# Kernel optimization log

Measured on AMD Instinct MI355X. Metric: run time of the kernel, lower is better.

## Reference

```python
import math
import jax, jax.numpy as jnp
import numpy as np

B, L, D, H = 2, 2048, 1024, 16
HD = D // H
EPS = 1e-6
ROPE_BASE = 10000.0


def setup_inputs() -> dict:
    key = jax.random.key(0)
    ks = jax.random.split(key, 6)
    s = 0.02
    return {
        "z_H_previous": jax.random.normal(ks[0], (B, L, D), jnp.float32),
        "z_L_current": jax.random.normal(ks[1], (B, L, D), jnp.float32),
        "w_qkv": jax.random.normal(ks[2], (3 * D, D), jnp.float32) * s,
        "w_out": jax.random.normal(ks[3], (D, D), jnp.float32) * s,
        "w_ffn1": jax.random.normal(ks[4], (4 * D, D), jnp.float32) * s,
        "w_ffn2": jax.random.normal(ks[5], (D, 4 * D), jnp.float32) * s,
        "g_norm1": jnp.ones((D,), jnp.float32),
        "g_norm2": jnp.ones((D,), jnp.float32),
    }


def _rmsnorm(x, g):
    # mean of squares over last dim, rsqrt, scale
    ms = jnp.mean(x * x, axis=-1, keepdims=True)
    return x * jax.lax.rsqrt(ms + EPS) * g


def _rope(x):
    # x: [b, h, l, hd]; non-interleaved rotate-half RoPE
    l, d = x.shape[-2], x.shape[-1]
    half = d // 2
    inv_freq = 1.0 / (ROPE_BASE ** (jnp.arange(half, dtype=jnp.float32) / half))
    freqs = jnp.arange(l, dtype=jnp.float32)[:, None] * inv_freq[None, :]  # [l, half]
    cos, sin = jnp.cos(freqs), jnp.sin(freqs)
    x1, x2 = x[..., :half], x[..., half:]
    return jnp.concatenate([x1 * cos - x2 * sin, x2 * cos + x1 * sin], axis=-1)


def reference(z_H_previous, z_L_current, w_qkv, w_out, w_ffn1, w_ffn2, g_norm1, g_norm2):
    x = z_H_previous + z_L_current                       # [b, l, d]
    h = _rmsnorm(x, g_norm1)
    b, l, d = h.shape
    qkv = h @ w_qkv.T                                    # [b, l, 3d]
    qkv = qkv.reshape(b, l, 3, H, HD).transpose(2, 0, 3, 1, 4)  # [3, b, h, l, hd]
    q, k, v = qkv[0], qkv[1], qkv[2]
    q = _rope(q)
    k = _rope(k)
    scores = jnp.einsum("bhqd,bhkd->bhqk", q, k) / math.sqrt(HD)
    attn = jax.nn.softmax(scores, axis=-1)
    out = jnp.einsum("bhqk,bhkd->bhqd", attn, v)         # [b, h, l, hd]
    out = out.transpose(0, 2, 1, 3).reshape(b, l, d)
    x = x + out @ w_out.T
    h2 = _rmsnorm(x, g_norm2)
    ffn = jax.nn.silu(h2 @ w_ffn1.T) @ w_ffn2.T
    return x + ffn
```

## Files before the change

### kernel.cpp

```cpp
#include <hip/hip_runtime.h>

typedef __bf16 bf16;
typedef __bf16 bf16x2 __attribute__((ext_vector_type(2)));
typedef __bf16 bf16x8 __attribute__((ext_vector_type(8)));
typedef __bf16 bf16x4 __attribute__((ext_vector_type(4)));
typedef float  f32x4  __attribute__((ext_vector_type(4)));
typedef float  f32x16 __attribute__((ext_vector_type(16)));
typedef unsigned int uint;

static __device__ __forceinline__ void async_copy16(const void* g, void* l) {
  __builtin_amdgcn_global_load_lds((__attribute__((address_space(1))) void*)g,
                                   (__attribute__((address_space(3))) void*)l,
                                   16, 0, 0);
}

static __device__ __forceinline__ uint pkbf2(float a, float b) {
  union { bf16x2 v; uint u; } x;
  x.v[0] = (bf16)a; x.v[1] = (bf16)b;
  return x.u;
}

union U4 { uint u[4]; bf16x8 v; };

__global__ __launch_bounds__(256) void f2b_kernel(const float* __restrict__ in,
                                                  bf16* __restrict__ out, int n4) {
  int i = blockIdx.x * 256 + threadIdx.x;
  if (i < n4) {
    float4 v = ((const float4*)in)[i];
    bf16x4 o;
    o[0] = (bf16)v.x; o[1] = (bf16)v.y; o[2] = (bf16)v.z; o[3] = (bf16)v.w;
    ((bf16x4*)out)[i] = o;
  }
}

__global__ __launch_bounds__(256)
void add_rmsnorm_kernel(const float* __restrict__ a, const float* __restrict__ b,
                        const float* __restrict__ g, float* __restrict__ xout,
                        bf16* __restrict__ hout) {
  const int row = blockIdx.x;
  const int tid = threadIdx.x;
  const size_t base = (size_t)row * 1024 + tid * 4;
  float4 x = *(const float4*)(a + base);
  if (b) {
    float4 y = *(const float4*)(b + base);
    x.x += y.x; x.y += y.y; x.z += y.z; x.w += y.w;
  }
  float ss = x.x*x.x + x.y*x.y + x.z*x.z + x.w*x.w;
#pragma unroll
  for (int off = 32; off > 0; off >>= 1) ss += __shfl_xor(ss, off, 64);
  __shared__ float red[4];
  const int wave = tid >> 6, lane = tid & 63;
  if (lane == 0) red[wave] = ss;
  __syncthreads();
  const float total = red[0] + red[1] + red[2] + red[3];
  const float scale = rsqrtf(total * (1.0f / 1024.0f) + 1e-6f);
  if (xout) *(float4*)(xout + base) = x;
  float4 gv = *(const float4*)(g + tid * 4);
  bf16x4 h;
  h[0] = (bf16)(x.x * scale * gv.x);
  h[1] = (bf16)(x.y * scale * gv.y);
  h[2] = (bf16)(x.z * scale * gv.z);
  h[3] = (bf16)(x.w * scale * gv.w);
  *(bf16x4*)(hout + base) = h;
}

__global__ __launch_bounds__(256) void rope_kernel(bf16* __restrict__ qk) {
  int idx = blockIdx.x * 256 + threadIdx.x;
  const int hd = idx & 31; idx >>= 5;
  const int l  = idx & 2047; idx >>= 11;
  const int h  = idx & 15; idx >>= 4;
  const int b  = idx & 1;  idx >>= 1;
  bf16* p = qk + (size_t)idx * 4194304 + ((size_t)(b * 16 + h) * 2048 + l) * 64;
  const float inv = powf(10000.0f, -(float)hd * (1.0f / 32.0f));
  const float fr = (float)l * inv;
  float s, c; sincosf(fr, &s, &c);
  const float x1 = (float)p[hd], x2 = (float)p[hd + 32];
  p[hd]      = (bf16)(x1 * c - x2 * s);
  p[hd + 32] = (bf16)(x2 * c + x1 * s);
}

enum { EP_QKV = 0, EP_ADD_RESID = 1, EP_SILU = 2 };

template <int MODE>
__global__ __launch_bounds__(256)
void gemm_bt(const bf16* __restrict__ A, const bf16* __restrict__ W,
             const float* __restrict__ resid, float* __restrict__ outF,
             bf16* __restrict__ outB, bf16* __restrict__ outB2,
             int M, int N, int K) {
  __shared__ bf16 As[128 * 32];
  __shared__ bf16 Bs[128 * 32];
  const int tid  = threadIdx.x;
  const int wave = tid >> 6;
  const int lane = tid & 63;
  const int quad = lane >> 4;
  const int l16  = lane & 15;

  const int nb = N >> 7;
  const int bm = blockIdx.x / nb;
  const int bn = blockIdx.x - bm * nb;
  const int m0 = bm << 7, n0 = bn << 7;
  const int wm = (wave >> 1) << 6;
  const int wn = (wave & 1) << 6;

  const int srow = wave * 32 + (lane >> 2);
  const int scol = (lane & 3) * 8;
  const bf16* gA = A + (size_t)(m0 + srow) * K + scol;
  const bf16* gB = W + (size_t)(n0 + srow) * K + scol;
  bf16* lA0 = &As[(wave * 32) * 32];
  bf16* lA1 = &As[(wave * 32 + 16) * 32];
  bf16* lB0 = &Bs[(wave * 32) * 32];
  bf16* lB1 = &Bs[(wave * 32 + 16) * 32];

  f32x4 acc[4][4] = {};

  for (int k0 = 0; k0 < K; k0 += 32) {
    __syncthreads();
    async_copy16(gA, lA0);
    async_copy16(gA + (size_t)16 * K, lA1);
    async_copy16(gB, lB0);
    async_copy16(gB + (size_t)16 * K, lB1);
    gA += 32; gB += 32;
    __syncthreads();
    bf16x8 af[4], bfr[4];
#pragma unroll
    for (int i = 0; i < 4; i++)
      af[i] = *(const bf16x8*)&As[(wm + i * 16 + l16) * 32 + quad * 8];
#pragma unroll
    for (int j = 0; j < 4; j++)
      bfr[j] = *(const bf16x8*)&Bs[(wn + j * 16 + l16) * 32 + quad * 8];
#pragma unroll
    for (int i = 0; i < 4; i++)
#pragma unroll
      for (int j = 0; j < 4; j++)
        acc[i][j] = __builtin_amdgcn_mfma_f32_16x16x32_bf16(af[i], bfr[j], acc[i][j], 0, 0, 0);
  }

#pragma unroll
  for (int i = 0; i < 4; i++) {
    const int mbase = m0 + wm + i * 16 + quad * 4;
#pragma unroll
    for (int j = 0; j < 4; j++) {
      const int n = n0 + wn + j * 16 + l16;
      f32x4 v = acc[i][j];
#pragma unroll
      for (int r = 0; r < 4; r++) {
        const int m = mbase + r;
        const float val = v[r];
        if constexpr (MODE == EP_QKV) {
          const int bb = m >> 11, l = m & 2047;
          const int which = n >> 10, hh = (n >> 6) & 15, hd = n & 63;
          if (which == 2) {
            outB2[((size_t)(bb * 16 + hh) * 64 + hd) * 2048 + l] = (bf16)val;
          } else {
            const float sc = (which == 0) ? 0.1803368801111243f : 1.0f;
            outB[(((size_t)(which * 2 + bb) * 16 + hh) * 2048 + l) * 64 + hd] = (bf16)(val * sc);
          }
        } else if constexpr (MODE == EP_ADD_RESID) {
          outF[(size_t)m * N + n] = val + resid[(size_t)m * N + n];
        } else {
          outB[(size_t)m * N + n] = (bf16)(val / (1.0f + __expf(-val)));
        }
      }
    }
  }
}

__global__ __launch_bounds__(256)
void gemm64_bt(const bf16* __restrict__ A, const bf16* __restrict__ W,
               const float* __restrict__ resid, float* __restrict__ outF,
               int M, int N, int K) {
  __shared__ bf16 As[64 * 32];
  __shared__ bf16 Bs[128 * 32];
  const int tid = threadIdx.x, wave = tid >> 6, lane = tid & 63;
  const int quad = lane >> 4, l16 = lane & 15;
  const int nb = N >> 7;
  const int bm = blockIdx.x / nb, bn = blockIdx.x - bm * nb;
  const int m0 = bm << 6, n0 = bn << 7;
  const int wm = (wave >> 1) * 32, wn = (wave & 1) * 64;

  const int arow = wave * 16 + (lane >> 2);
  const int brow = wave * 32 + (lane >> 2);
  const int scol = (lane & 3) * 8;
  const bf16* gA = A + (size_t)(m0 + arow) * K + scol;
  const bf16* gB = W + (size_t)(n0 + brow) * K + scol;
  bf16* lA  = &As[(wave * 16) * 32];
  bf16* lB0 = &Bs[(wave * 32) * 32];
  bf16* lB1 = &Bs[(wave * 32 + 16) * 32];

  f32x4 acc[2][4] = {};
  for (int k0 = 0; k0 < K; k0 += 32) {
    __syncthreads();
    async_copy16(gA, lA);
    async_copy16(gB, lB0);
    async_copy16(gB + (size_t)16 * K, lB1);
    gA += 32; gB += 32;
    __syncthreads();
    bf16x8 af[2], bfr[4];
#pragma unroll
    for (int i = 0; i < 2; i++)
      af[i] = *(const bf16x8*)&As[(wm + i * 16 + l16) * 32 + quad * 8];
#pragma unroll
    for (int j = 0; j < 4; j++)
      bfr[j] = *(const bf16x8*)&Bs[(wn + j * 16 + l16) * 32 + quad * 8];
#pragma unroll
    for (int i = 0; i < 2; i++)
#pragma unroll
      for (int j = 0; j < 4; j++)
        acc[i][j] = __builtin_amdgcn_mfma_f32_16x16x32_bf16(af[i], bfr[j], acc[i][j], 0, 0, 0);
  }
#pragma unroll
  for (int i = 0; i < 2; i++) {
    const int mbase = m0 + wm + i * 16 + quad * 4;
#pragma unroll
    for (int j = 0; j < 4; j++) {
      const int n = n0 + wn + j * 16 + l16;
#pragma unroll
      for (int r = 0; r < 4; r++) {
        const int m = mbase + r;
        outF[(size_t)m * N + n] = acc[i][j][r] + resid[(size_t)m * N + n];
      }
    }
  }
}

__global__ __launch_bounds__(256, 4)
void attn_kernel(const bf16* __restrict__ qk, const bf16* __restrict__ vt,
                 bf16* __restrict__ Opart, float* __restrict__ Lpart) {
  const int qt    = blockIdx.x & 15;
  const int bh    = (blockIdx.x >> 4) & 31;
  const int split = blockIdx.x >> 9;
  const bf16* Qp = qk + (size_t)bh * 131072;
  const bf16* Kp = Qp + 4194304;
  const bf16* Vp = vt + (size_t)bh * 131072;

  const int tid = threadIdx.x, wave = tid >> 6, lane = tid & 63;
  const int hl = lane >> 5, l32 = lane & 31;
  const int qw = qt * 128 + wave * 32;

  __shared__ bf16 lds[9216];
  bf16* Ks = lds;
  bf16* Vs = lds + 4096;

  bf16x8 qf[4];
#pragma unroll
  for (int dk = 0; dk < 4; dk++)
    qf[dk] = *(const bf16x8*)&Qp[(size_t)(qw + l32) * 64 + dk * 16 + hl * 8];

  f32x16 o0 = {}, o1 = {};
  float l_i = 0.0f;

  const int rl = lane >> 3;
  const int cg = (lane & 7) ^ rl;

  const int kvbase = split * 512;
  for (int kv0 = kvbase; kv0 < kvbase + 512; kv0 += 64) {
    __syncthreads();
#pragma unroll
    for (int i = 0; i < 2; i++) {
      const int row = wave * 16 + i * 8;
      async_copy16(Kp + (size_t)(kv0 + row + rl) * 64 + cg * 8, &Ks[row * 64]);
      async_copy16(Vp + (size_t)(row + rl) * 2048 + kv0 + cg * 8, &Vs[row * 64]);
    }
    __syncthreads();

    f32x16 s0 = {}, s1 = {};
#pragma unroll
    for (int dk = 0; dk < 4; dk++) {
      const bf16x8 kf = *(const bf16x8*)&Ks[l32 * 64 + ((dk * 2 + hl) ^ (l32 & 7)) * 8];
      s0 = __builtin_amdgcn_mfma_f32_32x32x16_bf16(kf, qf[dk], s0, 0, 0, 0);
    }
#pragma unroll
    for (int dk = 0; dk < 4; dk++) {
      const bf16x8 kf = *(const bf16x8*)&Ks[(32 + l32) * 64 + ((dk * 2 + hl) ^ (l32 & 7)) * 8];
      s1 = __builtin_amdgcn_mfma_f32_32x32x16_bf16(kf, qf[dk], s1, 0, 0, 0);
    }

    U4 pf[4];
    float sum = 0.0f;
#pragma unroll
    for (int ks = 0; ks < 2; ks++) {
      const f32x16 sv = ks ? s1 : s0;
      uint d[8];
#pragma unroll
      for (int i = 0; i < 8; i++) {
        const float a = exp2f(sv[2 * i]);
        const float b = exp2f(sv[2 * i + 1]);
        sum += a + b;
        d[i] = pkbf2(a, b);
      }
      uint send0 = hl ? d[0] : d[2];
      uint send1 = hl ? d[1] : d[3];
      uint send2 = hl ? d[4] : d[6];
      uint send3 = hl ? d[5] : d[7];
      const uint r0 = __shfl_xor(send0, 32, 64);
      const uint r1 = __shfl_xor(send1, 32, 64);
      const uint r2 = __shfl_xor(send2, 32, 64);
      const uint r3 = __shfl_xor(send3, 32, 64);
      U4& f0 = pf[ks * 2];
      U4& f1 = pf[ks * 2 + 1];
      f0.u[0] = hl ? r0 : d[0];  f0.u[1] = hl ? r1 : d[1];
      f0.u[2] = hl ? d[2] : r0;  f0.u[3] = hl ? d[3] : r1;
      f1.u[0] = hl ? r2 : d[4];  f1.u[1] = hl ? r3 : d[5];
      f1.u[2] = hl ? d[6] : r2;  f1.u[3] = hl ? d[7] : r3;
    }
    l_i += sum + __shfl_xor(sum, 32, 64);

#pragma unroll
    for (int c16 = 0; c16 < 4; c16++) {
      const bf16x8 vf0 = *(const bf16x8*)&Vs[l32 * 64 + ((c16 * 2 + hl) ^ (l32 & 7)) * 8];
      const bf16x8 vf1 = *(const bf16x8*)&Vs[(32 + l32) * 64 + ((c16 * 2 + hl) ^ (l32 & 7)) * 8];
      o0 = __builtin_amdgcn_mfma_f32_32x32x16_bf16(vf0, pf[c16].v, o0, 0, 0, 0);
      o1 = __builtin_amdgcn_mfma_f32_32x32x16_bf16(vf1, pf[c16].v, o1, 0, 0, 0);
    }
  }

  Lpart[(size_t)(split * 32 + bh) * 2048 + qt * 128 + wave * 32 + l32] = l_i;

  __syncthreads();
  uint* L32 = (uint*)lds;
  const int qloc = wave * 32 + l32;
#pragma unroll
  for (int ds = 0; ds < 2; ds++) {
    const f32x16 ov = ds ? o1 : o0;
#pragma unroll
    for (int i = 0; i < 8; i++) {
      const int r = 2 * i;
      const int dd = ds * 32 + (r & 3) + 8 * (r >> 2) + 4 * hl;
      L32[qloc * 36 + (dd >> 1)] = pkbf2(ov[r], ov[r + 1]);
    }
  }
  __syncthreads();
#pragma unroll
  for (int p = 0; p < 4; p++) {
    const int qr = p * 32 + (tid >> 3), c = tid & 7;
    const uint4 v = *(const uint4*)&L32[qr * 36 + c * 4];
    *(uint4*)&Opart[(((size_t)(split * 32 + bh) * 2048) + qt * 128 + qr) * 64 + c * 8] = v;
  }
}

__global__ __launch_bounds__(256)
void attn_combine(const bf16* __restrict__ Opart, const float* __restrict__ Lpart,
                  bf16* __restrict__ out) {
  const int t = blockIdx.x * 256 + threadIdx.x;
  const int c = t & 7, qq = t >> 3;
  const int bh = qq >> 11, q = qq & 2047;
  const int b = bh >> 4, h = bh & 15;
  float acc[8] = {};
  float lsum = 0.0f;
#pragma unroll
  for (int s = 0; s < 4; s++) {
    const bf16x8 ov = *(const bf16x8*)&Opart[((size_t)(s * 32 + bh) * 2048 + q) * 64 + c * 8];
    lsum += Lpart[(size_t)(s * 32 + bh) * 2048 + q];
#pragma unroll
    for (int i = 0; i < 8; i++) acc[i] += (float)ov[i];
  }
  const float inv = 1.0f / lsum;
  bf16x8 o;
#pragma unroll
  for (int i = 0; i < 8; i++) o[i] = (bf16)(acc[i] * inv);
  *(bf16x8*)&out[((size_t)b * 2048 + q) * 1024 + h * 64 + c * 8] = o;
}

extern "C" void kernel_launch(void* const* d_in, const int* in_sizes, int n_in,
                              void* d_out, int out_size, void* d_ws, size_t ws_size,
                              hipStream_t stream) {
  (void)in_sizes; (void)n_in; (void)out_size; (void)ws_size;
  const float* zH    = (const float*)d_in[0];
  const float* zL    = (const float*)d_in[1];
  const float* w_qkv = (const float*)d_in[2];
  const float* w_out = (const float*)d_in[3];
  const float* w_f1  = (const float*)d_in[4];
  const float* w_f2  = (const float*)d_in[5];
  const float* g1    = (const float*)d_in[6];
  const float* g2    = (const float*)d_in[7];
  float* out = (float*)d_out;

  char* ws = (char*)d_ws;
  size_t off = 0;
  auto alloc = [&](size_t bytes) {
    void* p = ws + off;
    off += (bytes + 255) & ~(size_t)255;
    return p;
  };
  bf16*  bqkv  = (bf16*)alloc(3145728ull * 2);
  bf16*  bwout = (bf16*)alloc(1048576ull * 2);
  bf16*  bf1   = (bf16*)alloc(4194304ull * 2);
  bf16*  bf2   = (bf16*)alloc(4194304ull * 2);
  float* x     = (float*)alloc(4194304ull * 4);
  bf16*  hbuf  = (bf16*)alloc(4194304ull * 2);
  bf16*  qkb   = (bf16*)alloc(8388608ull * 2);
  bf16*  vtb   = (bf16*)alloc(4194304ull * 2);
  bf16*  attnb = (bf16*)alloc(4194304ull * 2);
  const size_t offU = off;
  float* x2    = (float*)alloc(4194304ull * 4);
  bf16*  h2    = (bf16*)alloc(4194304ull * 2);
  bf16*  act   = (bf16*)alloc(16777216ull * 2);
  bf16*  Opart = (bf16*)(ws + offU);
  float* Lpart = (float*)(ws + offU + 16777216ull * 2 + 256);

  f2b_kernel<<<3072, 256, 0, stream>>>(w_qkv, bqkv, 3145728 / 4);
  f2b_kernel<<<1024, 256, 0, stream>>>(w_out, bwout, 1048576 / 4);
  f2b_kernel<<<4096, 256, 0, stream>>>(w_f1, bf1, 4194304 / 4);
  f2b_kernel<<<4096, 256, 0, stream>>>(w_f2, bf2, 4194304 / 4);

  add_rmsnorm_kernel<<<4096, 256, 0, stream>>>(zH, zL, g1, x, hbuf);

  gemm_bt<EP_QKV><<<768, 256, 0, stream>>>(hbuf, bqkv, nullptr, nullptr, qkb, vtb,
                                           4096, 3072, 1024);
  rope_kernel<<<16384, 256, 0, stream>>>(qkb);
  attn_kernel<<<2048, 256, 0, stream>>>(qkb, vtb, Opart, Lpart);
  attn_combine<<<2048, 256, 0, stream>>>(Opart, Lpart, attnb);

  gemm64_bt<<<512, 256, 0, stream>>>(attnb, bwout, x, x2, 4096, 1024, 1024);
  add_rmsnorm_kernel<<<4096, 256, 0, stream>>>(x2, nullptr, g2, nullptr, h2);
  gemm_bt<EP_SILU><<<1024, 256, 0, stream>>>(h2, bf1, nullptr, nullptr, act, nullptr,
                                             4096, 4096, 1024);
  gemm64_bt<<<512, 256, 0, stream>>>(act, bf2, x2, out, 4096, 1024, 4096);
}
```

Baseline: 428.9 us.

## Swizzle LDS tiles in GEMMs and split-K the FFN down-projection

```diff
diff --git a/kernel.cpp b/kernel.cpp
--- a/kernel.cpp
+++ b/kernel.cpp
@@ -103,7 +103,7 @@
   const int wn = (wave & 1) << 6;
 
   const int srow = wave * 32 + (lane >> 2);
-  const int scol = (lane & 3) * 8;
+  const int scol = (((lane & 3) ^ ((lane >> 3) & 3)) * 8);
   const bf16* gA = A + (size_t)(m0 + srow) * K + scol;
   const bf16* gB = W + (size_t)(n0 + srow) * K + scol;
   bf16* lA0 = &As[(wave * 32) * 32];
@@ -111,6 +111,7 @@
   bf16* lB0 = &Bs[(wave * 32) * 32];
   bf16* lB1 = &Bs[(wave * 32 + 16) * 32];
 
+  const int sw = (l16 >> 1) & 3;
   f32x4 acc[4][4] = {};
 
   for (int k0 = 0; k0 < K; k0 += 32) {
@@ -124,10 +125,10 @@
     bf16x8 af[4], bfr[4];
 #pragma unroll
     for (int i = 0; i < 4; i++)
-      af[i] = *(const bf16x8*)&As[(wm + i * 16 + l16) * 32 + quad * 8];
+      af[i] = *(const bf16x8*)&As[(wm + i * 16 + l16) * 32 + ((quad ^ sw) * 8)];
 #pragma unroll
     for (int j = 0; j < 4; j++)
-      bfr[j] = *(const bf16x8*)&Bs[(wn + j * 16 + l16) * 32 + quad * 8];
+      bfr[j] = *(const bf16x8*)&Bs[(wn + j * 16 + l16) * 32 + ((quad ^ sw) * 8)];
 #pragma unroll
     for (int i = 0; i < 4; i++)
 #pragma unroll
@@ -166,6 +167,91 @@
 }
 
 __global__ __launch_bounds__(256)
+void gemm_bt_splitk(const bf16* __restrict__ A, const bf16* __restrict__ W,
+                    float* __restrict__ P, int M, int N, int Ktot) {
+  __shared__ bf16 As[128 * 32];
+  __shared__ bf16 Bs[128 * 32];
+  const int tid  = threadIdx.x;
+  const int wave = tid >> 6;
+  const int lane = tid & 63;
+  const int quad = lane >> 4;
+  const int l16  = lane & 15;
+
+  const int nb = N >> 7;
+  const int tiles = (M >> 7) * nb;
+  const int t = blockIdx.x % tiles;
+  const int split = blockIdx.x / tiles;
+  const int bm = t / nb, bn = t - bm * nb;
+  const int m0 = bm << 7, n0 = bn << 7;
+  const int wm = (wave >> 1) << 6;
+  const int wn = (wave & 1) << 6;
+  const int Kh = Ktot >> 1;
+  const int koff = split * Kh;
+
+  const int srow = wave * 32 + (lane >> 2);
+  const int scol = (((lane & 3) ^ ((lane >> 3) & 3)) * 8);
+  const bf16* gA = A + (size_t)(m0 + srow) * Ktot + koff + scol;
+  const bf16* gB = W + (size_t)(n0 + srow) * Ktot + koff + scol;
+  bf16* lA0 = &As[(wave * 32) * 32];
+  bf16* lA1 = &As[(wave * 32 + 16) * 32];
+  bf16* lB0 = &Bs[(wave * 32) * 32];
+  bf16* lB1 = &Bs[(wave * 32 + 16) * 32];
+
+  const int sw = (l16 >> 1) & 3;
+  f32x4 acc[4][4] = {};
+
+  for (int k0 = 0; k0 < Kh; k0 += 32) {
+    __syncthreads();
+    async_copy16(gA, lA0);
+    async_copy16(gA + (size_t)16 * Ktot, lA1);
+    async_copy16(gB, lB0);
+    async_copy16(gB + (size_t)16 * Ktot, lB1);
+    gA += 32; gB += 32;
+    __syncthreads();
+    bf16x8 af[4], bfr[4];
+#pragma unroll
+    for (int i = 0; i < 4; i++)
+      af[i] = *(const bf16x8*)&As[(wm + i * 16 + l16) * 32 + ((quad ^ sw) * 8)];
+#pragma unroll
+    for (int j = 0; j < 4; j++)
+      bfr[j] = *(const bf16x8*)&Bs[(wn + j * 16 + l16) * 32 + ((quad ^ sw) * 8)];
+#pragma unroll
+    for (int i = 0; i < 4; i++)
+#pragma unroll
+      for (int j = 0; j < 4; j++)
+        acc[i][j] = __builtin_amdgcn_mfma_f32_16x16x32_bf16(af[i], bfr[j], acc[i][j], 0, 0, 0);
+  }
+
+  float* Pd = P + (size_t)split * M * N;
+#pragma unroll
+  for (int i = 0; i < 4; i++) {
+    const int mbase = m0 + wm + i * 16 + quad * 4;
+#pragma unroll
+    for (int j = 0; j < 4; j++) {
+      const int n = n0 + wn + j * 16 + l16;
+#pragma unroll
+      for (int r = 0; r < 4; r++)
+        Pd[(size_t)(mbase + r) * N + n] = acc[i][j][r];
+    }
+  }
+}
+
+__global__ __launch_bounds__(256)
+void splitk_combine(const float* __restrict__ P, const float* __restrict__ resid,
+                    float* __restrict__ out, int total4) {
+  int i = blockIdx.x * 256 + threadIdx.x;
+  if (i < total4) {
+    float4 a = ((const float4*)P)[i];
+    float4 b = ((const float4*)(P + 4194304))[i];
+    float4 r = ((const float4*)resid)[i];
+    float4 o;
+    o.x = a.x + b.x + r.x; o.y = a.y + b.y + r.y;
+    o.z = a.z + b.z + r.z; o.w = a.w + b.w + r.w;
+    ((float4*)out)[i] = o;
+  }
+}
+
+__global__ __launch_bounds__(256)
 void gemm64_bt(const bf16* __restrict__ A, const bf16* __restrict__ W,
                const float* __restrict__ resid, float* __restrict__ outF,
                int M, int N, int K) {
@@ -180,13 +266,14 @@
 
   const int arow = wave * 16 + (lane >> 2);
   const int brow = wave * 32 + (lane >> 2);
-  const int scol = (lane & 3) * 8;
+  const int scol = (((lane & 3) ^ ((lane >> 3) & 3)) * 8);
   const bf16* gA = A + (size_t)(m0 + arow) * K + scol;
   const bf16* gB = W + (size_t)(n0 + brow) * K + scol;
   bf16* lA  = &As[(wave * 16) * 32];
   bf16* lB0 = &Bs[(wave * 32) * 32];
   bf16* lB1 = &Bs[(wave * 32 + 16) * 32];
 
+  const int sw = (l16 >> 1) & 3;
   f32x4 acc[2][4] = {};
   for (int k0 = 0; k0 < K; k0 += 32) {
     __syncthreads();
@@ -198,10 +285,10 @@
     bf16x8 af[2], bfr[4];
 #pragma unroll
     for (int i = 0; i < 2; i++)
-      af[i] = *(const bf16x8*)&As[(wm + i * 16 + l16) * 32 + quad * 8];
+      af[i] = *(const bf16x8*)&As[(wm + i * 16 + l16) * 32 + ((quad ^ sw) * 8)];
 #pragma unroll
     for (int j = 0; j < 4; j++)
-      bfr[j] = *(const bf16x8*)&Bs[(wn + j * 16 + l16) * 32 + quad * 8];
+      bfr[j] = *(const bf16x8*)&Bs[(wn + j * 16 + l16) * 32 + ((quad ^ sw) * 8)];
 #pragma unroll
     for (int i = 0; i < 2; i++)
 #pragma unroll
@@ -386,6 +473,7 @@
   bf16*  bwout = (bf16*)alloc(1048576ull * 2);
   bf16*  bf1   = (bf16*)alloc(4194304ull * 2);
   bf16*  bf2   = (bf16*)alloc(4194304ull * 2);
+  const size_t off_x = off;
   float* x     = (float*)alloc(4194304ull * 4);
   bf16*  hbuf  = (bf16*)alloc(4194304ull * 2);
   bf16*  qkb   = (bf16*)alloc(8388608ull * 2);
@@ -397,6 +485,7 @@
   bf16*  act   = (bf16*)alloc(16777216ull * 2);
   bf16*  Opart = (bf16*)(ws + offU);
   float* Lpart = (float*)(ws + offU + 16777216ull * 2 + 256);
+  float* Ppart = (float*)(ws + off_x);
 
   f2b_kernel<<<3072, 256, 0, stream>>>(w_qkv, bqkv, 3145728 / 4);
   f2b_kernel<<<1024, 256, 0, stream>>>(w_out, bwout, 1048576 / 4);
@@ -415,5 +504,6 @@
   add_rmsnorm_kernel<<<4096, 256, 0, stream>>>(x2, nullptr, g2, nullptr, h2);
   gemm_bt<EP_SILU><<<1024, 256, 0, stream>>>(h2, bf1, nullptr, nullptr, act, nullptr,
                                              4096, 4096, 1024);
-  gemm64_bt<<<512, 256, 0, stream>>>(act, bf2, x2, out, 4096, 1024, 4096);
-}
+  gemm_bt_splitk<<<512, 256, 0, stream>>>(act, bf2, Ppart, 4096, 1024, 4096);
+  splitk_combine<<<4096, 256, 0, stream>>>(Ppart, x2, out, 1048576);
+}
```

New measurement: 420.1 us. 1.02x faster.
